# Kernel tuning notes

Measured on AMD Instinct MI355X. Metric: run time of the kernel, lower is better.

## Reference

```python
import jax, jax.numpy as jnp
import numpy as np

N = 100000   # nodes
E = 1600000  # edges
D = 128      # input_dim == hidden_dim
L = 3        # n_layers
P = 7        # n_properties
B = 64       # graphs in batch
BN_EPS = 1e-5
NEG_SLOPE = 0.2


def setup_inputs() -> dict:
    key = jax.random.key(0)
    ks = jax.random.split(key, 18)
    s = 1.0 / np.sqrt(D)
    sp = 1.0 / np.sqrt(P)
    return {
        "x": jax.random.normal(ks[0], (N, D), jnp.float32),
        "edge_index": jax.random.randint(ks[1], (2, E), 0, N, dtype=jnp.int64),
        "batch": jnp.sort(jax.random.randint(ks[2], (N,), 0, B, dtype=jnp.int64)),
        "graph_stats": jax.random.normal(ks[3], (B, P), jnp.float32),
        # GIN MLP params (stacked over layers; input_dim == hidden_dim == D)
        "W1s": jax.random.normal(ks[4], (L, D, D), jnp.float32) * s,
        "b1s": jnp.zeros((L, D), jnp.float32),
        "gammas": jnp.ones((L, D), jnp.float32),
        "betas": jnp.zeros((L, D), jnp.float32),
        "bn_means": jax.random.normal(ks[5], (L, D), jnp.float32) * 0.1,
        "bn_vars": jax.random.uniform(ks[6], (L, D), jnp.float32) + 0.5,
        "W2s": jax.random.normal(ks[7], (L, D, D), jnp.float32) * s,
        "b2s": jnp.zeros((L, D), jnp.float32),
        # stat conditioning transforms
        "statWs": jax.random.normal(ks[8], (L, P, D), jnp.float32) * sp,
        "statBs": jnp.zeros((L, D), jnp.float32),
        # fc_out
        "fcW": jax.random.normal(ks[9], (D, D), jnp.float32) * s,
        "fcB": jnp.zeros((D,), jnp.float32),
    }


def reference(x, edge_index, batch, graph_stats,
              W1s, b1s, gammas, betas, bn_means, bn_vars, W2s, b2s,
              statWs, statBs, fcW, fcB):
    # per-node graph stats (nan -> -100, then broadcast by graph id)
    node_stats = jnp.nan_to_num(graph_stats, nan=-100.0)[batch]  # [N, P]
    src, dst = edge_index[0], edge_index[1]
    h = x
    for i in range(L):
        # GIN aggregation (eps = 0): (1+eps)*h_i + sum_{j->i} h_j
        agg = jax.ops.segment_sum(h[src], dst, num_segments=N)  # [N, D]
        m = h + agg
        # MLP: Linear -> LeakyReLU(0.2) -> BatchNorm1d (eval) -> Linear -> LeakyReLU(0.2)
        m = jax.nn.leaky_relu(m @ W1s[i] + b1s[i], NEG_SLOPE)
        m = (m - bn_means[i]) * (gammas[i] / jnp.sqrt(bn_vars[i] + BN_EPS)) + betas[i]
        m = jax.nn.leaky_relu(m @ W2s[i] + b2s[i], NEG_SLOPE)
        # stats conditioning add (dropout is identity in eval mode)
        h = m + node_stats @ statWs[i] + statBs[i]
    return h @ fcW + fcB  # [N, D]
```

## Files before the change

kernel.cpp:

```cpp
#include <hip/hip_runtime.h>
#include <math.h>

#define N_NODES 100000
#define N_EDGES 1600000
#define D 128
#define L_LAYERS 3
#define P_STATS 7
#define B_GRAPHS 64
#define BN_EPS 1e-5f
#define NEG_SLOPE 0.2f

#define NB 196
#define BCAP 10240
#define EPB 6400

typedef __attribute__((ext_vector_type(8))) short bf16x8;
typedef __attribute__((ext_vector_type(4))) float f32x4;

static __device__ __forceinline__ short f2bf(float f) {
    union { float f; unsigned u; } v;
    v.f = f;
    unsigned r = v.u + 0x7fffu + ((v.u >> 16) & 1u);
    return (short)(r >> 16);
}

static __device__ __forceinline__ float bf2f(short s) {
    union { unsigned u; float f; } v;
    v.u = ((unsigned)(unsigned short)s) << 16;
    return v.f;
}


__global__ void zero_n_kernel(int* __restrict__ p, int n) {
    int i = blockIdx.x * blockDim.x + threadIdx.x;
    if (i < n) p[i] = 0;
}

__global__ __launch_bounds__(256) void bucketA_kernel(const int* __restrict__ src,
                                                      const int* __restrict__ dst,
                                                      int* __restrict__ bucket_cnt,
                                                      int2* __restrict__ bucketbuf) {
    __shared__ int hist[NB], base[NB], loc[NB];
    const int tid = threadIdx.x;
    const int e0 = blockIdx.x * EPB;
    for (int i = tid; i < NB; i += 256) { hist[i] = 0; loc[i] = 0; }
    __syncthreads();
    for (int i = tid; i < EPB; i += 256) {
        int d = dst[e0 + i];
        atomicAdd(&hist[d >> 9], 1);
    }
    __syncthreads();
    for (int i = tid; i < NB; i += 256)
        base[i] = hist[i] ? atomicAdd(&bucket_cnt[i], hist[i]) : 0;
    __syncthreads();
    for (int i = tid; i < EPB; i += 256) {
        int s = src[e0 + i];
        int d = dst[e0 + i];
        int b = d >> 9;
        int off = atomicAdd(&loc[b], 1);
        int idx = base[b] + off;
        if (idx < BCAP) bucketbuf[(size_t)b * BCAP + idx] = make_int2(s, d);
    }
}

__global__ __launch_bounds__(256) void bucketB1_kernel(const int* __restrict__ bucket_cnt,
                                                       const int2* __restrict__ bucketbuf,
                                                       int* __restrict__ deg) {
    __shared__ int hist[512];
    const int b = blockIdx.x;
    for (int i = threadIdx.x; i < 512; i += 256) hist[i] = 0;
    __syncthreads();
    int cnt = min(bucket_cnt[b], BCAP);
    for (int i = threadIdx.x; i < cnt; i += 256) {
        int d = bucketbuf[(size_t)b * BCAP + i].y;
        atomicAdd(&hist[d & 511], 1);
    }
    __syncthreads();
    int nbase = b << 9;
    for (int i = threadIdx.x; i < 512; i += 256) {
        int node = nbase + i;
        if (node < N_NODES) deg[node] = hist[i];
    }
}

__global__ __launch_bounds__(256) void bucketB2_kernel(const int* __restrict__ bucket_cnt,
                                                       const int2* __restrict__ bucketbuf,
                                                       int* __restrict__ cursor,
                                                       int* __restrict__ csr_src) {
    const int b = blockIdx.x;
    int cnt = min(bucket_cnt[b], BCAP);
    for (int i = threadIdx.x; i < cnt; i += 256) {
        int2 p = bucketbuf[(size_t)b * BCAP + i];
        int pos = atomicAdd(&cursor[p.y], 1);
        csr_src[pos] = p.x;
    }
}


__global__ void scan1_kernel(const int* __restrict__ deg, int* __restrict__ incl,
                             int* __restrict__ bsum) {
    __shared__ int s[256];
    const int tid = threadIdx.x;
    const int base = blockIdx.x * 2048;
    int v[8];
    int sum = 0;
    const int idx0 = base + tid * 8;
#pragma unroll
    for (int i = 0; i < 8; ++i) {
        int idx = idx0 + i;
        int d = (idx < N_NODES) ? deg[idx] : 0;
        sum += d;
        v[i] = sum;
    }
    s[tid] = sum;
    __syncthreads();
    for (int off = 1; off < 256; off <<= 1) {
        int t = (tid >= off) ? s[tid - off] : 0;
        __syncthreads();
        s[tid] += t;
        __syncthreads();
    }
    int prev = (tid > 0) ? s[tid - 1] : 0;
#pragma unroll
    for (int i = 0; i < 8; ++i) {
        int idx = idx0 + i;
        if (idx < N_NODES) incl[idx] = v[i] + prev;
    }
    if (tid == 255) bsum[blockIdx.x] = s[255];
}

__global__ void scan2_kernel(int* __restrict__ bsum, int nb) {
    if (threadIdx.x == 0 && blockIdx.x == 0) {
        int run = 0;
        for (int i = 0; i < nb; ++i) { int t = bsum[i]; bsum[i] = run; run += t; }
    }
}

__global__ void scan3_kernel(const int* __restrict__ deg, const int* __restrict__ incl,
                             const int* __restrict__ bsum, int* __restrict__ start,
                             int* __restrict__ cursor) {
    int i = blockIdx.x * blockDim.x + threadIdx.x;
    if (i < N_NODES) {
        int inc = incl[i] + bsum[i >> 11];
        int st = inc - deg[i];
        start[i] = st;
        cursor[i] = st;
    }
    if (i == 0) start[N_NODES] = N_EDGES;
}

__global__ void gproj_kernel(const float* __restrict__ gs, const float* __restrict__ statWs,
                             const float* __restrict__ statBs, float* __restrict__ gproj) {
    int b = blockIdx.x;
    int l = blockIdx.y;
    int j = threadIdx.x;
    float acc = statBs[l * D + j];
#pragma unroll
    for (int p = 0; p < P_STATS; ++p) {
        float g = gs[b * P_STATS + p];
        if (g != g) g = -100.0f;
        acc += g * statWs[(l * P_STATS + p) * D + j];
    }
    gproj[(l * B_GRAPHS + b) * D + j] = acc;
}

__global__ void wconv_kernel(const float* __restrict__ W1s, const float* __restrict__ W2s,
                             const float* __restrict__ fcW, short* __restrict__ wt) {
    int mid = blockIdx.y;
    const float* src = (mid < 3) ? (W1s + mid * D * D)
                                 : ((mid < 6) ? (W2s + (mid - 3) * D * D) : fcW);
    short* dstm = wt + mid * D * D;
    int i = blockIdx.x * 256 + threadIdx.x;
    int k = i >> 7, n = i & 127;
    dstm[n * D + k] = f2bf(src[i]);
}

__global__ __launch_bounds__(256) void agg_ep_kernel(const short* __restrict__ g,
                                                     const int* __restrict__ start,
                                                     const int* __restrict__ csr_src,
                                                     const float* __restrict__ b1,
                                                     const float* __restrict__ gamma,
                                                     const float* __restrict__ beta,
                                                     const float* __restrict__ mean,
                                                     const float* __restrict__ var,
                                                     short* __restrict__ z) {
    int node = blockIdx.x * 16 + (threadIdx.x >> 4);
    int c8 = threadIdx.x & 15;
    const bf16x8* g8 = (const bf16x8*)g;

    bf16x8 own = g8[node * 16 + c8];
    float acc[8];
#pragma unroll
    for (int i = 0; i < 8; ++i) acc[i] = bf2f(own[i]);

    int s = start[node];
    int e = start[node + 1];
    int k = s;
    for (; k + 4 <= e; k += 4) {
        int sn0 = csr_src[k];
        int sn1 = csr_src[k + 1];
        int sn2 = csr_src[k + 2];
        int sn3 = csr_src[k + 3];
        bf16x8 v0 = g8[sn0 * 16 + c8];
        bf16x8 v1 = g8[sn1 * 16 + c8];
        bf16x8 v2 = g8[sn2 * 16 + c8];
        bf16x8 v3 = g8[sn3 * 16 + c8];
#pragma unroll
        for (int i = 0; i < 8; ++i) acc[i] += bf2f(v0[i]);
#pragma unroll
        for (int i = 0; i < 8; ++i) acc[i] += bf2f(v1[i]);
#pragma unroll
        for (int i = 0; i < 8; ++i) acc[i] += bf2f(v2[i]);
#pragma unroll
        for (int i = 0; i < 8; ++i) acc[i] += bf2f(v3[i]);
    }
    for (; k < e; ++k) {
        int sn0 = csr_src[k];
        bf16x8 v0 = g8[sn0 * 16 + c8];
#pragma unroll
        for (int i = 0; i < 8; ++i) acc[i] += bf2f(v0[i]);
    }

    const int f0 = c8 * 8;
    float4 bb0 = *(const float4*)&b1[f0];
    float4 bb1 = *(const float4*)&b1[f0 + 4];
    float4 gm0 = *(const float4*)&gamma[f0];
    float4 gm1 = *(const float4*)&gamma[f0 + 4];
    float4 bt0 = *(const float4*)&beta[f0];
    float4 bt1 = *(const float4*)&beta[f0 + 4];
    float4 mn0 = *(const float4*)&mean[f0];
    float4 mn1 = *(const float4*)&mean[f0 + 4];
    float4 vr0 = *(const float4*)&var[f0];
    float4 vr1 = *(const float4*)&var[f0 + 4];
    float bbv[8] = {bb0.x, bb0.y, bb0.z, bb0.w, bb1.x, bb1.y, bb1.z, bb1.w};
    float gmv[8] = {gm0.x, gm0.y, gm0.z, gm0.w, gm1.x, gm1.y, gm1.z, gm1.w};
    float btv[8] = {bt0.x, bt0.y, bt0.z, bt0.w, bt1.x, bt1.y, bt1.z, bt1.w};
    float mnv[8] = {mn0.x, mn0.y, mn0.z, mn0.w, mn1.x, mn1.y, mn1.z, mn1.w};
    float vrv[8] = {vr0.x, vr0.y, vr0.z, vr0.w, vr1.x, vr1.y, vr1.z, vr1.w};

    short pk[8];
#pragma unroll
    for (int i = 0; i < 8; ++i) {
        float t = acc[i] + bbv[i];
        t = (t > 0.f) ? t : NEG_SLOPE * t;
        float sc = gmv[i] * rsqrtf(vrv[i] + BN_EPS);
        t = t * sc + (btv[i] - mnv[i] * sc);
        pk[i] = f2bf(t);
    }
    *(bf16x8*)&z[node * D + f0] = *(bf16x8*)pk;
}

__global__ __launch_bounds__(256, 4) void initgemm_kernel(const float* __restrict__ x,
                                                          const short* __restrict__ Wt,
                                                          short* __restrict__ g_out) {
    __shared__ short sy[64 * 128];
    const int tid = threadIdx.x;
    const int wid = tid >> 6;
    const int lane = tid & 63;
    const int lr = lane & 15;
    const int lk = lane >> 4;

    const int nlBase = (wid >> 1) * 32;
    const int nodeBase = blockIdx.x * 64 + nlBase;
    const int featBase = (wid & 1) * 64;

    int nIdx[2];
#pragma unroll
    for (int mt = 0; mt < 2; ++mt) {
        int n = nodeBase + mt * 16 + lr;
        nIdx[mt] = (n < N_NODES) ? n : (N_NODES - 1);
    }

    f32x4 acc[4][2];
#pragma unroll
    for (int ft = 0; ft < 4; ++ft)
#pragma unroll
        for (int mt = 0; mt < 2; ++mt)
            acc[ft][mt] = (f32x4)(0.0f);

#pragma unroll
    for (int kt = 0; kt < 4; ++kt) {
        bf16x8 wfk[4];
#pragma unroll
        for (int ft = 0; ft < 4; ++ft)
            wfk[ft] = *(const bf16x8*)&Wt[(featBase + ft * 16 + lr) * D + kt * 32 + lk * 8];
        bf16x8 mf[2];
#pragma unroll
        for (int mt = 0; mt < 2; ++mt) {
            const float4* xp = (const float4*)&x[nIdx[mt] * D + kt * 32 + lk * 8];
            float4 a = xp[0], b = xp[1];
            short q[8];
            q[0] = f2bf(a.x); q[1] = f2bf(a.y); q[2] = f2bf(a.z); q[3] = f2bf(a.w);
            q[4] = f2bf(b.x); q[5] = f2bf(b.y); q[6] = f2bf(b.z); q[7] = f2bf(b.w);
            mf[mt] = *(bf16x8*)q;
        }
#pragma unroll
        for (int ft = 0; ft < 4; ++ft)
#pragma unroll
            for (int mt = 0; mt < 2; ++mt)
                acc[ft][mt] = __builtin_amdgcn_mfma_f32_16x16x32_bf16(wfk[ft], mf[mt],
                                                                      acc[ft][mt], 0, 0, 0);
    }

#pragma unroll
    for (int ft = 0; ft < 4; ++ft) {
        int f0 = featBase + ft * 16 + lk * 4;
#pragma unroll
        for (int mt = 0; mt < 2; ++mt) {
            int nl = nlBase + mt * 16 + lr;
            short4 pk;
#pragma unroll
            for (int r = 0; r < 4; ++r) ((short*)&pk)[r] = f2bf(acc[ft][mt][r]);
            int byteoff = nl * 256 + f0 * 2;
            byteoff ^= (nl & 7) << 4;
            *(short4*)((char*)sy + byteoff) = pk;
        }
    }
    __syncthreads();
#pragma unroll
    for (int it = 0; it < 4; ++it) {
        int c = tid + it * 256;
        int nl = c >> 4;
        int c8 = c & 15;
        int node = blockIdx.x * 64 + nl;
        if (node < N_NODES) {
            int byteoff = nl * 256 + c8 * 16;
            byteoff ^= (nl & 7) << 4;
            bf16x8 v = *(const bf16x8*)((char*)sy + byteoff);
            *(bf16x8*)&g_out[node * D + c8 * 8] = v;
        }
    }
}

template <bool FINAL>
__global__ __launch_bounds__(256, 4) void mlp2_kernel(
    const short* __restrict__ z,
    const short* __restrict__ W2t,
    const float* __restrict__ b2,
    const float* __restrict__ gproj, const int* __restrict__ batch,
    const short* __restrict__ Wnt,
    const float* __restrict__ fcb,
    float* __restrict__ outf, short* __restrict__ g_out) {
    __shared__ short sy[64 * 128];
    __shared__ float sB2[128], sFC[128];

    const int tid = threadIdx.x;
    const int wid = tid >> 6;
    const int lane = tid & 63;
    const int lr = lane & 15;
    const int lk = lane >> 4;

    if (tid < 128) {
        sB2[tid] = b2[tid];
        if (FINAL) sFC[tid] = fcb[tid];
    }
    __syncthreads();

    const int nlBase = (wid >> 1) * 32;
    const int nodeBase = blockIdx.x * 64 + nlBase;
    const int featBase = (wid & 1) * 64;

    int nIdx[2];
#pragma unroll
    for (int mt = 0; mt < 2; ++mt) {
        int n = nodeBase + mt * 16 + lr;
        nIdx[mt] = (n < N_NODES) ? n : (N_NODES - 1);
    }

    f32x4 acc[4][2];
#pragma unroll
    for (int ft = 0; ft < 4; ++ft)
#pragma unroll
        for (int mt = 0; mt < 2; ++mt)
            acc[ft][mt] = (f32x4)(0.0f);

#pragma unroll
    for (int kt = 0; kt < 4; ++kt) {
        bf16x8 wfk[4];
#pragma unroll
        for (int ft = 0; ft < 4; ++ft)
            wfk[ft] = *(const bf16x8*)&W2t[(featBase + ft * 16 + lr) * D + kt * 32 + lk * 8];
        bf16x8 zf[2];
#pragma unroll
        for (int mt = 0; mt < 2; ++mt)
            zf[mt] = *(const bf16x8*)&z[nIdx[mt] * D + kt * 32 + lk * 8];
#pragma unroll
        for (int ft = 0; ft < 4; ++ft)
#pragma unroll
            for (int mt = 0; mt < 2; ++mt)
                acc[ft][mt] = __builtin_amdgcn_mfma_f32_16x16x32_bf16(wfk[ft], zf[mt],
                                                                      acc[ft][mt], 0, 0, 0);
    }

#pragma unroll
    for (int ft = 0; ft < 4; ++ft) {
        int f0 = featBase + ft * 16 + lk * 4;
#pragma unroll
        for (int mt = 0; mt < 2; ++mt) {
            int nl = nlBase + mt * 16 + lr;
            int bid = batch[nIdx[mt]];
            const float4 gp = *(const float4*)&gproj[bid * D + f0];
            short4 pk;
            float v0 = acc[ft][mt][0] + sB2[f0 + 0]; v0 = (v0 > 0.f) ? v0 : NEG_SLOPE * v0; v0 += gp.x;
            float v1 = acc[ft][mt][1] + sB2[f0 + 1]; v1 = (v1 > 0.f) ? v1 : NEG_SLOPE * v1; v1 += gp.y;
            float v2 = acc[ft][mt][2] + sB2[f0 + 2]; v2 = (v2 > 0.f) ? v2 : NEG_SLOPE * v2; v2 += gp.z;
            float v3 = acc[ft][mt][3] + sB2[f0 + 3]; v3 = (v3 > 0.f) ? v3 : NEG_SLOPE * v3; v3 += gp.w;
            pk.x = f2bf(v0); pk.y = f2bf(v1); pk.z = f2bf(v2); pk.w = f2bf(v3);
            int byteoff = nl * 256 + f0 * 2;
            byteoff ^= (nl & 7) << 4;
            *(short4*)((char*)sy + byteoff) = pk;
        }
    }
    __syncthreads();

#pragma unroll
    for (int ft = 0; ft < 4; ++ft)
#pragma unroll
        for (int mt = 0; mt < 2; ++mt)
            acc[ft][mt] = (f32x4)(0.0f);

#pragma unroll
    for (int kt = 0; kt < 4; ++kt) {
        bf16x8 wfk[4];
#pragma unroll
        for (int ft = 0; ft < 4; ++ft)
            wfk[ft] = *(const bf16x8*)&Wnt[(featBase + ft * 16 + lr) * D + kt * 32 + lk * 8];
        bf16x8 hf[2];
#pragma unroll
        for (int mt = 0; mt < 2; ++mt) {
            int nl = nlBase + mt * 16 + lr;
            int byteoff = nl * 256 + kt * 64 + lk * 16;
            byteoff ^= (nl & 7) << 4;
            hf[mt] = *(const bf16x8*)((char*)sy + byteoff);
        }
#pragma unroll
        for (int ft = 0; ft < 4; ++ft)
#pragma unroll
            for (int mt = 0; mt < 2; ++mt)
                acc[ft][mt] = __builtin_amdgcn_mfma_f32_16x16x32_bf16(wfk[ft], hf[mt],
                                                                      acc[ft][mt], 0, 0, 0);
    }

    if (FINAL) {
#pragma unroll
        for (int mt = 0; mt < 2; ++mt) {
            int node = nodeBase + mt * 16 + lr;
            if (node >= N_NODES) continue;
#pragma unroll
            for (int ft = 0; ft < 4; ++ft) {
                int f0 = featBase + ft * 16 + lk * 4;
                float4 o;
                o.x = acc[ft][mt][0] + sFC[f0 + 0];
                o.y = acc[ft][mt][1] + sFC[f0 + 1];
                o.z = acc[ft][mt][2] + sFC[f0 + 2];
                o.w = acc[ft][mt][3] + sFC[f0 + 3];
                *(float4*)&outf[node * D + f0] = o;
            }
        }
        return;
    }

    __syncthreads();
#pragma unroll
    for (int ft = 0; ft < 4; ++ft) {
        int f0 = featBase + ft * 16 + lk * 4;
#pragma unroll
        for (int mt = 0; mt < 2; ++mt) {
            int nl = nlBase + mt * 16 + lr;
            short4 pk;
#pragma unroll
            for (int r = 0; r < 4; ++r) ((short*)&pk)[r] = f2bf(acc[ft][mt][r]);
            int byteoff = nl * 256 + f0 * 2;
            byteoff ^= (nl & 7) << 4;
            *(short4*)((char*)sy + byteoff) = pk;
        }
    }
    __syncthreads();
#pragma unroll
    for (int it = 0; it < 4; ++it) {
        int c = tid + it * 256;
        int nl = c >> 4;
        int c8 = c & 15;
        int node = blockIdx.x * 64 + nl;
        if (node < N_NODES) {
            int byteoff = nl * 256 + c8 * 16;
            byteoff ^= (nl & 7) << 4;
            bf16x8 v = *(const bf16x8*)((char*)sy + byteoff);
            *(bf16x8*)&g_out[node * D + c8 * 8] = v;
        }
    }
}


extern "C" void kernel_launch(void* const* d_in, const int* in_sizes, int n_in,
                              void* d_out, int out_size, void* d_ws, size_t ws_size,
                              hipStream_t stream) {
    const float* x = (const float*)d_in[0];
    const int* ei = (const int*)d_in[1];
    const int* src = ei;
    const int* dst = ei + N_EDGES;
    const int* batch = (const int*)d_in[2];
    const float* gs = (const float*)d_in[3];
    const float* W1s = (const float*)d_in[4];
    const float* b1s = (const float*)d_in[5];
    const float* gammas = (const float*)d_in[6];
    const float* betas = (const float*)d_in[7];
    const float* means = (const float*)d_in[8];
    const float* vars = (const float*)d_in[9];
    const float* W2s = (const float*)d_in[10];
    const float* b2s = (const float*)d_in[11];
    const float* statWs = (const float*)d_in[12];
    const float* statBs = (const float*)d_in[13];
    const float* fcW = (const float*)d_in[14];
    const float* fcB = (const float*)d_in[15];
    float* out = (float*)d_out;

    char* ws = (char*)d_ws;
    auto alloc = [&](size_t bytes) {
        char* p = ws;
        ws += (bytes + 255) / 256 * 256;
        return p;
    };
    int* deg = (int*)alloc(N_NODES * sizeof(int));
    int* incl = (int*)alloc(N_NODES * sizeof(int));
    int* bsum = (int*)alloc(64 * sizeof(int));
    int* start = (int*)alloc((N_NODES + 1) * sizeof(int));
    int* cursor = (int*)alloc(N_NODES * sizeof(int));
    int* csr_src = (int*)alloc(N_EDGES * sizeof(int));
    int* bucket_cnt = (int*)alloc(NB * sizeof(int));
    int2* bucketbuf = (int2*)alloc((size_t)NB * BCAP * sizeof(int2));
    float* gproj = (float*)alloc((size_t)L_LAYERS * B_GRAPHS * D * sizeof(float));
    short* wt = (short*)alloc((size_t)7 * D * D * sizeof(short));
    short* g_buf = (short*)alloc((size_t)N_NODES * D * sizeof(short));
    short* z_buf = (short*)alloc((size_t)N_NODES * D * sizeof(short));

    const int nscan = (N_NODES + 2047) / 2048;

    zero_n_kernel<<<1, 256, 0, stream>>>(bucket_cnt, NB);
    bucketA_kernel<<<N_EDGES / EPB, 256, 0, stream>>>(src, dst, bucket_cnt, bucketbuf);
    bucketB1_kernel<<<NB, 256, 0, stream>>>(bucket_cnt, bucketbuf, deg);
    scan1_kernel<<<nscan, 256, 0, stream>>>(deg, incl, bsum);
    scan2_kernel<<<1, 64, 0, stream>>>(bsum, nscan);
    scan3_kernel<<<(N_NODES + 255) / 256, 256, 0, stream>>>(deg, incl, bsum, start, cursor);
    bucketB2_kernel<<<NB, 256, 0, stream>>>(bucket_cnt, bucketbuf, cursor, csr_src);

    gproj_kernel<<<dim3(B_GRAPHS, L_LAYERS), D, 0, stream>>>(gs, statWs, statBs, gproj);
    wconv_kernel<<<dim3(64, 7), 256, 0, stream>>>(W1s, W2s, fcW, wt);

    const int agg_blocks = N_NODES / 16;
    const int mlp_blocks = (N_NODES + 63) / 64;

    initgemm_kernel<<<mlp_blocks, 256, 0, stream>>>(x, wt + 0 * D * D, g_buf);

    agg_ep_kernel<<<agg_blocks, 256, 0, stream>>>(g_buf, start, csr_src, b1s + 0 * D,
                                                  gammas + 0 * D, betas + 0 * D, means + 0 * D,
                                                  vars + 0 * D, z_buf);
    mlp2_kernel<false><<<mlp_blocks, 256, 0, stream>>>(
        z_buf, wt + 3 * D * D, b2s + 0 * D, gproj + 0 * B_GRAPHS * D, batch,
        wt + 1 * D * D, nullptr, nullptr, g_buf);
    agg_ep_kernel<<<agg_blocks, 256, 0, stream>>>(g_buf, start, csr_src, b1s + 1 * D,
                                                  gammas + 1 * D, betas + 1 * D, means + 1 * D,
                                                  vars + 1 * D, z_buf);
    mlp2_kernel<false><<<mlp_blocks, 256, 0, stream>>>(
        z_buf, wt + 4 * D * D, b2s + 1 * D, gproj + 1 * B_GRAPHS * D, batch,
        wt + 2 * D * D, nullptr, nullptr, g_buf);
    agg_ep_kernel<<<agg_blocks, 256, 0, stream>>>(g_buf, start, csr_src, b1s + 2 * D,
                                                  gammas + 2 * D, betas + 2 * D, means + 2 * D,
                                                  vars + 2 * D, z_buf);
    mlp2_kernel<true><<<mlp_blocks, 256, 0, stream>>>(
        z_buf, wt + 5 * D * D, b2s + 2 * D, gproj + 2 * B_GRAPHS * D, batch,
        wt + 6 * D * D, fcB, out, nullptr);
}
```

Baseline: 429.9 us.

## Fuse CSR build into single bucket kernel with local scan and merged setup

Replaces the separate degree histogram, three-pass global scan, and scatter kernels with one per-bucket kernel. Each block computes its base offset by summing the preceding bucket counts, scans its 512 local node degrees in shared memory, and scatters sources using shared-memory cursors instead of global atomics. Edges are packed into a single int (src<<9 | dst&511) to halve bucket buffer traffic. The weight conversion, stat projection and counter zeroing are merged into one setup kernel. Together these cut the number of kernel launches and the global memory passes. The packing assumes src fits in 23 bits, which holds for 100k nodes.

Result: faster. 385.4 us (-10.3%).

```diff
diff --git a/kernel.cpp b/kernel.cpp
--- a/kernel.cpp
+++ b/kernel.cpp
@@ -30,16 +30,48 @@
     return v.f;
 }
 
-
-__global__ void zero_n_kernel(int* __restrict__ p, int n) {
-    int i = blockIdx.x * blockDim.x + threadIdx.x;
-    if (i < n) p[i] = 0;
+__global__ __launch_bounds__(256) void setup_kernel(const float* __restrict__ W1s,
+                                                    const float* __restrict__ W2s,
+                                                    const float* __restrict__ fcW,
+                                                    short* __restrict__ wt,
+                                                    const float* __restrict__ gs,
+                                                    const float* __restrict__ statWs,
+                                                    const float* __restrict__ statBs,
+                                                    float* __restrict__ gproj,
+                                                    int* __restrict__ bucket_cnt) {
+    const int bid = blockIdx.x;
+    const int tid = threadIdx.x;
+    if (bid < 448) {
+        int mid = bid >> 6;
+        int chunk = bid & 63;
+        const float* src = (mid < 3) ? (W1s + mid * D * D)
+                                     : ((mid < 6) ? (W2s + (mid - 3) * D * D) : fcW);
+        short* dstm = wt + mid * D * D;
+        int i = chunk * 256 + tid;
+        int k = i >> 7, n = i & 127;
+        dstm[n * D + k] = f2bf(src[i]);
+    } else if (bid < 448 + 96) {
+        int p = (bid - 448) * 2 + (tid >> 7);
+        int j = tid & 127;
+        int b = p & 63;
+        int l = p >> 6;
+        float acc = statBs[l * D + j];
+#pragma unroll
+        for (int q = 0; q < P_STATS; ++q) {
+            float g = gs[b * P_STATS + q];
+            if (g != g) g = -100.0f;
+            acc += g * statWs[(l * P_STATS + q) * D + j];
+        }
+        gproj[(l * B_GRAPHS + b) * D + j] = acc;
+    } else {
+        if (tid < NB) bucket_cnt[tid] = 0;
+    }
 }
 
 __global__ __launch_bounds__(256) void bucketA_kernel(const int* __restrict__ src,
                                                       const int* __restrict__ dst,
                                                       int* __restrict__ bucket_cnt,
-                                                      int2* __restrict__ bucketbuf) {
+                                                      int* __restrict__ bucketbuf) {
     __shared__ int hist[NB], base[NB], loc[NB];
     const int tid = threadIdx.x;
     const int e0 = blockIdx.x * EPB;
@@ -59,120 +91,66 @@
         int b = d >> 9;
         int off = atomicAdd(&loc[b], 1);
         int idx = base[b] + off;
-        if (idx < BCAP) bucketbuf[(size_t)b * BCAP + idx] = make_int2(s, d);
-    }
-}
-
-__global__ __launch_bounds__(256) void bucketB1_kernel(const int* __restrict__ bucket_cnt,
-                                                       const int2* __restrict__ bucketbuf,
-                                                       int* __restrict__ deg) {
+        if (idx < BCAP) bucketbuf[(size_t)b * BCAP + idx] = (s << 9) | (d & 511);
+    }
+}
+
+__global__ __launch_bounds__(256) void bucketB_kernel(const int* __restrict__ bucket_cnt,
+                                                      const int* __restrict__ bucketbuf,
+                                                      int* __restrict__ start,
+                                                      int* __restrict__ csr_src) {
     __shared__ int hist[512];
+    __shared__ int incl[512];
+    __shared__ int cursor[512];
+    __shared__ int red[256];
+    __shared__ int sbase_sh;
     const int b = blockIdx.x;
-    for (int i = threadIdx.x; i < 512; i += 256) hist[i] = 0;
-    __syncthreads();
-    int cnt = min(bucket_cnt[b], BCAP);
-    for (int i = threadIdx.x; i < cnt; i += 256) {
-        int d = bucketbuf[(size_t)b * BCAP + i].y;
-        atomicAdd(&hist[d & 511], 1);
-    }
-    __syncthreads();
-    int nbase = b << 9;
-    for (int i = threadIdx.x; i < 512; i += 256) {
-        int node = nbase + i;
-        if (node < N_NODES) deg[node] = hist[i];
-    }
-}
-
-__global__ __launch_bounds__(256) void bucketB2_kernel(const int* __restrict__ bucket_cnt,
-                                                       const int2* __restrict__ bucketbuf,
-                                                       int* __restrict__ cursor,
-                                                       int* __restrict__ csr_src) {
-    const int b = blockIdx.x;
-    int cnt = min(bucket_cnt[b], BCAP);
-    for (int i = threadIdx.x; i < cnt; i += 256) {
-        int2 p = bucketbuf[(size_t)b * BCAP + i];
-        int pos = atomicAdd(&cursor[p.y], 1);
-        csr_src[pos] = p.x;
-    }
-}
-
-
-__global__ void scan1_kernel(const int* __restrict__ deg, int* __restrict__ incl,
-                             int* __restrict__ bsum) {
-    __shared__ int s[256];
     const int tid = threadIdx.x;
-    const int base = blockIdx.x * 2048;
-    int v[8];
-    int sum = 0;
-    const int idx0 = base + tid * 8;
-#pragma unroll
-    for (int i = 0; i < 8; ++i) {
-        int idx = idx0 + i;
-        int d = (idx < N_NODES) ? deg[idx] : 0;
-        sum += d;
-        v[i] = sum;
-    }
-    s[tid] = sum;
-    __syncthreads();
-    for (int off = 1; off < 256; off <<= 1) {
-        int t = (tid >= off) ? s[tid - off] : 0;
+    const int cnt_b = min(bucket_cnt[b], BCAP);
+
+    int partial = 0;
+    for (int i = tid; i < b; i += 256) partial += min(bucket_cnt[i], BCAP);
+    red[tid] = partial;
+    __syncthreads();
+    for (int off = 128; off > 0; off >>= 1) {
+        if (tid < off) red[tid] += red[tid + off];
         __syncthreads();
-        s[tid] += t;
+    }
+    if (tid == 0) sbase_sh = red[0];
+
+    hist[tid] = 0;
+    hist[tid + 256] = 0;
+    __syncthreads();
+    const int* bb = bucketbuf + (size_t)b * BCAP;
+    for (int i = tid; i < cnt_b; i += 256) atomicAdd(&hist[bb[i] & 511], 1);
+    __syncthreads();
+    incl[tid] = hist[tid];
+    incl[tid + 256] = hist[tid + 256];
+    __syncthreads();
+    for (int off = 1; off < 512; off <<= 1) {
+        int i1 = tid + 256;
+        int v0 = (tid >= off) ? incl[tid - off] : 0;
+        int v1 = (i1 >= off) ? incl[i1 - off] : 0;
         __syncthreads();
-    }
-    int prev = (tid > 0) ? s[tid - 1] : 0;
-#pragma unroll
-    for (int i = 0; i < 8; ++i) {
-        int idx = idx0 + i;
-        if (idx < N_NODES) incl[idx] = v[i] + prev;
-    }
-    if (tid == 255) bsum[blockIdx.x] = s[255];
-}
-
-__global__ void scan2_kernel(int* __restrict__ bsum, int nb) {
-    if (threadIdx.x == 0 && blockIdx.x == 0) {
-        int run = 0;
-        for (int i = 0; i < nb; ++i) { int t = bsum[i]; bsum[i] = run; run += t; }
-    }
-}
-
-__global__ void scan3_kernel(const int* __restrict__ deg, const int* __restrict__ incl,
-                             const int* __restrict__ bsum, int* __restrict__ start,
-                             int* __restrict__ cursor) {
-    int i = blockIdx.x * blockDim.x + threadIdx.x;
-    if (i < N_NODES) {
-        int inc = incl[i] + bsum[i >> 11];
-        int st = inc - deg[i];
-        start[i] = st;
-        cursor[i] = st;
-    }
-    if (i == 0) start[N_NODES] = N_EDGES;
-}
-
-__global__ void gproj_kernel(const float* __restrict__ gs, const float* __restrict__ statWs,
-                             const float* __restrict__ statBs, float* __restrict__ gproj) {
-    int b = blockIdx.x;
-    int l = blockIdx.y;
-    int j = threadIdx.x;
-    float acc = statBs[l * D + j];
-#pragma unroll
-    for (int p = 0; p < P_STATS; ++p) {
-        float g = gs[b * P_STATS + p];
-        if (g != g) g = -100.0f;
-        acc += g * statWs[(l * P_STATS + p) * D + j];
-    }
-    gproj[(l * B_GRAPHS + b) * D + j] = acc;
-}
-
-__global__ void wconv_kernel(const float* __restrict__ W1s, const float* __restrict__ W2s,
-                             const float* __restrict__ fcW, short* __restrict__ wt) {
-    int mid = blockIdx.y;
-    const float* src = (mid < 3) ? (W1s + mid * D * D)
-                                 : ((mid < 6) ? (W2s + (mid - 3) * D * D) : fcW);
-    short* dstm = wt + mid * D * D;
-    int i = blockIdx.x * 256 + threadIdx.x;
-    int k = i >> 7, n = i & 127;
-    dstm[n * D + k] = f2bf(src[i]);
+        incl[tid] += v0;
+        incl[i1] += v1;
+        __syncthreads();
+    }
+    const int sbase = sbase_sh;
+    int excl0 = incl[tid] - hist[tid];
+    int excl1 = incl[tid + 256] - hist[tid + 256];
+    cursor[tid] = excl0;
+    cursor[tid + 256] = excl1;
+    const int nbase = b << 9;
+    if (nbase + tid < N_NODES) start[nbase + tid] = sbase + excl0;
+    if (nbase + tid + 256 < N_NODES) start[nbase + tid + 256] = sbase + excl1;
+    if (b == NB - 1 && tid == 0) start[N_NODES] = sbase + incl[511];
+    __syncthreads();
+    for (int i = tid; i < cnt_b; i += 256) {
+        int e = bb[i];
+        int pos = atomicAdd(&cursor[e & 511], 1);
+        csr_src[sbase + pos] = e >> 9;
+    }
 }
 
 __global__ __launch_bounds__(256) void agg_ep_kernel(const short* __restrict__ g,
@@ -521,31 +499,19 @@
         ws += (bytes + 255) / 256 * 256;
         return p;
     };
-    int* deg = (int*)alloc(N_NODES * sizeof(int));
-    int* incl = (int*)alloc(N_NODES * sizeof(int));
-    int* bsum = (int*)alloc(64 * sizeof(int));
     int* start = (int*)alloc((N_NODES + 1) * sizeof(int));
-    int* cursor = (int*)alloc(N_NODES * sizeof(int));
     int* csr_src = (int*)alloc(N_EDGES * sizeof(int));
     int* bucket_cnt = (int*)alloc(NB * sizeof(int));
-    int2* bucketbuf = (int2*)alloc((size_t)NB * BCAP * sizeof(int2));
+    int* bucketbuf = (int*)alloc((size_t)NB * BCAP * sizeof(int));
     float* gproj = (float*)alloc((size_t)L_LAYERS * B_GRAPHS * D * sizeof(float));
     short* wt = (short*)alloc((size_t)7 * D * D * sizeof(short));
     short* g_buf = (short*)alloc((size_t)N_NODES * D * sizeof(short));
     short* z_buf = (short*)alloc((size_t)N_NODES * D * sizeof(short));
 
-    const int nscan = (N_NODES + 2047) / 2048;
-
-    zero_n_kernel<<<1, 256, 0, stream>>>(bucket_cnt, NB);
+    setup_kernel<<<545, 256, 0, stream>>>(W1s, W2s, fcW, wt, gs, statWs, statBs, gproj,
+                                          bucket_cnt);
     bucketA_kernel<<<N_EDGES / EPB, 256, 0, stream>>>(src, dst, bucket_cnt, bucketbuf);
-    bucketB1_kernel<<<NB, 256, 0, stream>>>(bucket_cnt, bucketbuf, deg);
-    scan1_kernel<<<nscan, 256, 0, stream>>>(deg, incl, bsum);
-    scan2_kernel<<<1, 64, 0, stream>>>(bsum, nscan);
-    scan3_kernel<<<(N_NODES + 255) / 256, 256, 0, stream>>>(deg, incl, bsum, start, cursor);
-    bucketB2_kernel<<<NB, 256, 0, stream>>>(bucket_cnt, bucketbuf, cursor, csr_src);
-
-    gproj_kernel<<<dim3(B_GRAPHS, L_LAYERS), D, 0, stream>>>(gs, statWs, statBs, gproj);
-    wconv_kernel<<<dim3(64, 7), 256, 0, stream>>>(W1s, W2s, fcW, wt);
+    bucketB_kernel<<<NB, 256, 0, stream>>>(bucket_cnt, bucketbuf, start, csr_src);
 
     const int agg_blocks = N_NODES / 16;
     const int mlp_blocks = (N_NODES + 63) / 64;
```
